# Optimization experiments

Hardware: AMD Instinct MI355X
Metric: run time of the kernel (lower is better)

## Reference

```python
import jax, jax.numpy as jnp
import numpy as np

B, S, D_IN, D_Q, D_K = 4, 4096, 1024, 128, 128


def setup_inputs() -> dict:
    key = jax.random.key(0)
    ks = jax.random.split(key, 9)
    inv = 1.0 / np.sqrt(D_IN)
    return {
        "query": jax.random.normal(ks[0], (B, S, D_IN), dtype=jnp.float32),
        "key": jax.random.normal(ks[1], (B, S, D_IN), dtype=jnp.float32),
        "value": jax.random.normal(ks[2], (B, S, D_IN), dtype=jnp.float32),
        "Wq": jax.random.uniform(ks[3], (D_IN, D_Q), jnp.float32, -inv, inv),
        "bq": jax.random.uniform(ks[4], (D_Q,), jnp.float32, -inv, inv),
        "Wk": jax.random.uniform(ks[5], (D_IN, D_K), jnp.float32, -inv, inv),
        "bk": jax.random.uniform(ks[6], (D_K,), jnp.float32, -inv, inv),
        "Wv": jax.random.uniform(ks[7], (D_IN, D_K), jnp.float32, -inv, inv),
        "bv": jax.random.uniform(ks[8], (D_K,), jnp.float32, -inv, inv),
    }


def reference(query, key, value, Wq, bq, Wk, bk, Wv, bv):
    q = query @ Wq + bq          # [B,S,Dq]
    k = key @ Wk + bk            # [B,S,Dk]
    v = value @ Wv + bv          # [B,S,Dk]
    scale = 1.0 / jnp.sqrt(jnp.asarray(q.shape[-1], q.dtype))
    logits = jnp.einsum('bqd,bkd->bqk', q, k) * scale  # [B,S,S]
    attn = jax.nn.softmax(logits, axis=-1)
    return jnp.einsum('bqk,bkd->bqd', attn, v)         # [B,S,Dk]
```

## Files before the change

kernel.cpp:

```cpp
#include <hip/hip_runtime.h>
#include <hip/hip_bf16.h>


typedef __attribute__((ext_vector_type(8))) short v8s;
typedef __attribute__((ext_vector_type(4))) float v4f;
typedef __attribute__((ext_vector_type(2))) unsigned int v2u;
typedef __attribute__((ext_vector_type(4))) int v4i;

#define SEQ   4096
#define DIN   1024
#define DH    128
#define NBAT  4

__device__ __forceinline__ unsigned short f2bf(float f) {
  unsigned u = __float_as_uint(f);
  u += 0x7fffu + ((u >> 16) & 1u);
  return (unsigned short)(u >> 16);
}

__global__ void prep_weights(const float* __restrict__ Wq, const float* __restrict__ Wk,
                             const float* __restrict__ Wv, short* __restrict__ Wt) {
  int idx = blockIdx.x * 256 + threadIdx.x;
  int z = idx >> 17;
  int e = idx & 131071;
  int k = e >> 7, c = e & 127;
  const float* W = (z == 0) ? Wq : (z == 1) ? Wk : Wv;
  Wt[z * 131072 + c * 1024 + k] = (short)f2bf(W[e]);
}

__global__ __launch_bounds__(256) void qkv_proj(
    const float* __restrict__ Xq, const float* __restrict__ Xk, const float* __restrict__ Xv,
    const float* __restrict__ bq, const float* __restrict__ bk, const float* __restrict__ bv,
    const short* __restrict__ Wt,
    short* __restrict__ Qb, short* __restrict__ Kb, short* __restrict__ Vtb) {
  const int z = blockIdx.y;
  const float* X    = (z == 0) ? Xq : (z == 1) ? Xk : Xv;
  const float* bias = (z == 0) ? bq : (z == 1) ? bk : bv;
  const short* W    = Wt + z * 131072;

  const int tid = threadIdx.x, wid = tid >> 6, lane = tid & 63;
  const int lg = lane >> 4, li = lane & 15;
  const int r0 = blockIdx.x * 128 + wid * 32;

  const float* xp0 = X + (size_t)(r0 + li) * DIN + lg * 8;
  const float* xp1 = xp0 + (size_t)16 * DIN;

  v4f acc[2][8];
#pragma unroll
  for (int mi = 0; mi < 2; ++mi)
#pragma unroll
    for (int ni = 0; ni < 8; ++ni) { acc[mi][ni][0]=0.f; acc[mi][ni][1]=0.f; acc[mi][ni][2]=0.f; acc[mi][ni][3]=0.f; }

#pragma unroll 2
  for (int ks = 0; ks < 32; ++ks) {
    v4f x0 = *(const v4f*)(xp0 + ks * 32);
    v4f x1 = *(const v4f*)(xp0 + ks * 32 + 4);
    v4f y0 = *(const v4f*)(xp1 + ks * 32);
    v4f y1 = *(const v4f*)(xp1 + ks * 32 + 4);
    v8s a0, a1;
    a0[0]=(short)f2bf(x0[0]); a0[1]=(short)f2bf(x0[1]); a0[2]=(short)f2bf(x0[2]); a0[3]=(short)f2bf(x0[3]);
    a0[4]=(short)f2bf(x1[0]); a0[5]=(short)f2bf(x1[1]); a0[6]=(short)f2bf(x1[2]); a0[7]=(short)f2bf(x1[3]);
    a1[0]=(short)f2bf(y0[0]); a1[1]=(short)f2bf(y0[1]); a1[2]=(short)f2bf(y0[2]); a1[3]=(short)f2bf(y0[3]);
    a1[4]=(short)f2bf(y1[0]); a1[5]=(short)f2bf(y1[1]); a1[6]=(short)f2bf(y1[2]); a1[7]=(short)f2bf(y1[3]);
#pragma unroll
    for (int ni = 0; ni < 8; ++ni) {
      v8s b = *(const v8s*)&W[(ni * 16 + li) * DIN + ks * 32 + lg * 8];
      acc[0][ni] = __builtin_amdgcn_mfma_f32_16x16x32_bf16(a0, b, acc[0][ni], 0, 0, 0);
      acc[1][ni] = __builtin_amdgcn_mfma_f32_16x16x32_bf16(a1, b, acc[1][ni], 0, 0, 0);
    }
  }

#pragma unroll
  for (int ni = 0; ni < 8; ++ni) {
    const int col = ni * 16 + li;
    const float bb = bias[col];
#pragma unroll
    for (int mi = 0; mi < 2; ++mi) {
      const int row0 = r0 + mi * 16 + lg * 4;
      v4f r = acc[mi][ni];
      if (z < 2) {
        short* Out = (z == 0) ? Qb : Kb;
#pragma unroll
        for (int rr = 0; rr < 4; ++rr)
          Out[(size_t)(row0 + rr) * DH + col] = (short)f2bf(r[rr] + bb);
      } else {
        const int bat = row0 >> 12;
        const int s0  = row0 & 4095;
        unsigned lo = (unsigned)f2bf(r[0] + bb) | ((unsigned)f2bf(r[1] + bb) << 16);
        unsigned hi = (unsigned)f2bf(r[2] + bb) | ((unsigned)f2bf(r[3] + bb) << 16);
        v2u pk; pk[0] = lo; pk[1] = hi;
        *(v2u*)&Vtb[(size_t)bat * (DH * SEQ) + (size_t)col * SEQ + s0] = pk;
      }
    }
  }
}

template <int NSPLIT>
__global__ __launch_bounds__(256) void attn_fwd(
    const short* __restrict__ Qb, const short* __restrict__ Kb, const short* __restrict__ Vtb,
    float* __restrict__ out, float* __restrict__ Opart,
    float* __restrict__ Mpart, float* __restrict__ Lpart) {
  constexpr int SLEN = SEQ / NSPLIT;
  constexpr int NT = SLEN / 64;
  __shared__ __align__(16) short Kl[2][64 * 128];
  __shared__ __align__(16) short Vl[2][128 * 64];
  __shared__ __align__(16) short Pl[4][32 * 64];

  const int tid = threadIdx.x, wid = tid >> 6, lane = tid & 63;
  const int lg = lane >> 4, li = lane & 15;
  const int b = blockIdx.y;
  const int sp = (NSPLIT > 1) ? blockIdx.z : 0;
  const int q0 = blockIdx.x * 128 + wid * 32;
  const float kSc = 0.08838834764831845f * 1.4426950408889634f;
  const int swz = (li & 7) << 4;

  const char* Kp = (const char*)(Kb + ((size_t)b * SEQ + (size_t)sp * SLEN) * DH);
  const char* Vp = (const char*)(Vtb + (size_t)b * (DH * SEQ) + (size_t)sp * SLEN);
  const short* Q = Qb + ((size_t)b * SEQ + q0) * DH;
  char* myP = (char*)&Pl[wid][0];

  v8s qf[4][2];
#pragma unroll
  for (int dc = 0; dc < 4; ++dc)
#pragma unroll
    for (int qh = 0; qh < 2; ++qh)
      qf[dc][qh] = *(const v8s*)&Q[(size_t)(qh * 16 + li) * DH + dc * 32 + lg * 8];

  v4f o[8][2];
#pragma unroll
  for (int dt = 0; dt < 8; ++dt)
#pragma unroll
    for (int qh = 0; qh < 2; ++qh) { o[dt][qh][0]=0.f; o[dt][qh][1]=0.f; o[dt][qh][2]=0.f; o[dt][qh][3]=0.f; }
  float m[2] = {-1e30f, -1e30f}, l[2] = {0.f, 0.f};

  v4i kreg[4], vreg[4];
  auto loadKV = [&](int st0) {
#pragma unroll
    for (int j = 0; j < 4; ++j) {
      int c = tid + j * 256;
      kreg[j] = *(const v4i*)(Kp + (size_t)st0 * 256 + c * 16);
    }
#pragma unroll
    for (int j = 0; j < 4; ++j) {
      int c = tid + j * 256;
      int d = c >> 3;
      vreg[j] = *(const v4i*)(Vp + (size_t)d * (SEQ * 2) + st0 * 2 + (c & 7) * 16);
    }
  };
  auto writeKV = [&](int buf) {
    char* kb = (char*)&Kl[buf][0];
    char* vb = (char*)&Vl[buf][0];
#pragma unroll
    for (int j = 0; j < 4; ++j) {
      int lin = (tid + j * 256) * 16;
      *(v4i*)(kb + (lin ^ (((lin >> 8) & 7) << 4))) = kreg[j];
    }
#pragma unroll
    for (int j = 0; j < 4; ++j) {
      int lin = (tid + j * 256) * 16;
      *(v4i*)(vb + (lin ^ (((lin >> 7) & 7) << 4))) = vreg[j];
    }
  };

  loadKV(0);
  writeKV(0);

#pragma unroll 1
  for (int t = 0; t < NT; ++t) {
    __syncthreads();
    const int buf = t & 1;
    if (t + 1 < NT) loadKV((t + 1) * 64);
    const char* kb = (const char*)&Kl[buf][0];
    const char* vb = (const char*)&Vl[buf][0];

    v4f stt[4][2];
#pragma unroll
    for (int tt = 0; tt < 4; ++tt)
#pragma unroll
      for (int qh = 0; qh < 2; ++qh) { stt[tt][qh][0]=0.f; stt[tt][qh][1]=0.f; stt[tt][qh][2]=0.f; stt[tt][qh][3]=0.f; }
#pragma unroll
    for (int tt = 0; tt < 4; ++tt)
#pragma unroll
      for (int dc = 0; dc < 4; ++dc) {
        v8s kf = *(const v8s*)(kb + ((((tt * 16 + li) * 256) + dc * 64 + lg * 16) ^ swz));
        stt[tt][0] = __builtin_amdgcn_mfma_f32_16x16x32_bf16(kf, qf[dc][0], stt[tt][0], 0, 0, 0);
        stt[tt][1] = __builtin_amdgcn_mfma_f32_16x16x32_bf16(kf, qf[dc][1], stt[tt][1], 0, 0, 0);
      }

    float fac[2];
#pragma unroll
    for (int qh = 0; qh < 2; ++qh) {
      float mx = m[qh];
#pragma unroll
      for (int tt = 0; tt < 4; ++tt)
        mx = fmaxf(mx, fmaxf(fmaxf(stt[tt][qh][0], stt[tt][qh][1]), fmaxf(stt[tt][qh][2], stt[tt][qh][3])));
      mx = fmaxf(mx, __shfl_xor(mx, 16));
      mx = fmaxf(mx, __shfl_xor(mx, 32));
      fac[qh] = exp2f((m[qh] - mx) * kSc);
      m[qh] = mx;
      float ps = 0.f;
#pragma unroll
      for (int tt = 0; tt < 4; ++tt) {
        float p0 = exp2f((stt[tt][qh][0] - mx) * kSc);
        float p1 = exp2f((stt[tt][qh][1] - mx) * kSc);
        float p2 = exp2f((stt[tt][qh][2] - mx) * kSc);
        float p3 = exp2f((stt[tt][qh][3] - mx) * kSc);
        ps += (p0 + p1) + (p2 + p3);
        v2u pk;
        pk[0] = (unsigned)f2bf(p0) | ((unsigned)f2bf(p1) << 16);
        pk[1] = (unsigned)f2bf(p2) | ((unsigned)f2bf(p3) << 16);
        *(v2u*)(myP + ((((qh * 16 + li) * 128) + tt * 32 + lg * 8) ^ swz)) = pk;
      }
      ps += __shfl_xor(ps, 16);
      ps += __shfl_xor(ps, 32);
      l[qh] = l[qh] * fac[qh] + ps;
    }

    float facr[2][4];
#pragma unroll
    for (int qh = 0; qh < 2; ++qh)
#pragma unroll
      for (int r = 0; r < 4; ++r) facr[qh][r] = __shfl(fac[qh], lg * 4 + r);
#pragma unroll
    for (int dt = 0; dt < 8; ++dt)
#pragma unroll
      for (int qh = 0; qh < 2; ++qh) {
        o[dt][qh][0] *= facr[qh][0]; o[dt][qh][1] *= facr[qh][1];
        o[dt][qh][2] *= facr[qh][2]; o[dt][qh][3] *= facr[qh][3];
      }

#pragma unroll
    for (int kk = 0; kk < 2; ++kk) {
      v8s pf0 = *(const v8s*)(myP + (((li * 128) + kk * 64 + lg * 16) ^ swz));
      v8s pf1 = *(const v8s*)(myP + ((((16 + li) * 128) + kk * 64 + lg * 16) ^ swz));
#pragma unroll
      for (int dt = 0; dt < 8; ++dt) {
        v8s vf = *(const v8s*)(vb + ((((dt * 16 + li) * 128) + kk * 64 + lg * 16) ^ swz));
        o[dt][0] = __builtin_amdgcn_mfma_f32_16x16x32_bf16(pf0, vf, o[dt][0], 0, 0, 0);
        o[dt][1] = __builtin_amdgcn_mfma_f32_16x16x32_bf16(pf1, vf, o[dt][1], 0, 0, 0);
      }
    }

    if (t + 1 < NT) writeKV(buf ^ 1);
  }

  float lr[2][4];
#pragma unroll
  for (int qh = 0; qh < 2; ++qh)
#pragma unroll
    for (int r = 0; r < 4; ++r) lr[qh][r] = __shfl(l[qh], lg * 4 + r);

  if (NSPLIT == 1) {
#pragma unroll
    for (int dt = 0; dt < 8; ++dt)
#pragma unroll
      for (int qh = 0; qh < 2; ++qh)
#pragma unroll
        for (int r = 0; r < 4; ++r)
          out[((size_t)b * SEQ + q0 + qh * 16 + lg * 4 + r) * DH + dt * 16 + li] =
              o[dt][qh][r] / lr[qh][r];
  } else {
    const size_t rb = ((size_t)sp * NBAT + b) * SEQ + q0;
#pragma unroll
    for (int dt = 0; dt < 8; ++dt)
#pragma unroll
      for (int qh = 0; qh < 2; ++qh)
#pragma unroll
        for (int r = 0; r < 4; ++r)
          Opart[(rb + qh * 16 + lg * 4 + r) * DH + dt * 16 + li] = o[dt][qh][r];
    if (lg == 0) {
#pragma unroll
      for (int qh = 0; qh < 2; ++qh) {
        Mpart[rb + qh * 16 + li] = m[qh];
        Lpart[rb + qh * 16 + li] = l[qh];
      }
    }
  }
}

template <int NSPLIT>
__global__ void merge_out(const float* __restrict__ Opart, const float* __restrict__ Mpart,
                          const float* __restrict__ Lpart, float* __restrict__ out) {
  const float kSc = 0.08838834764831845f * 1.4426950408889634f;
  int idx = blockIdx.x * 256 + threadIdx.x;
  int row = idx >> 7;
  float M = -1e30f;
#pragma unroll
  for (int zz = 0; zz < NSPLIT; ++zz) M = fmaxf(M, Mpart[zz * (NBAT * SEQ) + row]);
  float num = 0.f, den = 0.f;
#pragma unroll
  for (int zz = 0; zz < NSPLIT; ++zz) {
    float w = exp2f((Mpart[zz * (NBAT * SEQ) + row] - M) * kSc);
    num += w * Opart[(size_t)zz * ((size_t)NBAT * SEQ * DH) + idx];
    den += w * Lpart[zz * (NBAT * SEQ) + row];
  }
  out[idx] = num / den;
}

extern "C" void kernel_launch(void* const* d_in, const int* in_sizes, int n_in,
                              void* d_out, int out_size, void* d_ws, size_t ws_size,
                              hipStream_t stream) {
  const float* query = (const float*)d_in[0];
  const float* key   = (const float*)d_in[1];
  const float* value = (const float*)d_in[2];
  const float* Wq    = (const float*)d_in[3];
  const float* bqp   = (const float*)d_in[4];
  const float* Wk    = (const float*)d_in[5];
  const float* bkp   = (const float*)d_in[6];
  const float* Wv    = (const float*)d_in[7];
  const float* bvp   = (const float*)d_in[8];

  char* ws = (char*)d_ws;
  const size_t WT_SZ  = (size_t)3 * 128 * 1024 * 2;
  const size_t QKV_SZ = (size_t)NBAT * SEQ * DH * 2;
  short* Wt  = (short*)ws;
  short* Qb  = (short*)(ws + WT_SZ);
  short* Kb  = (short*)(ws + WT_SZ + QKV_SZ);
  short* Vtb = (short*)(ws + WT_SZ + 2 * QKV_SZ);
  char*  ext = ws + WT_SZ + 3 * QKV_SZ;
  const size_t OP4 = (size_t)4 * NBAT * SEQ * DH * 4;
  const size_t ST4 = (size_t)4 * NBAT * SEQ * 4;
  const size_t OP2 = OP4 / 2, ST2 = ST4 / 2;
  const size_t need4 = WT_SZ + 3 * QKV_SZ + OP4 + 2 * ST4;
  const size_t need2 = WT_SZ + 3 * QKV_SZ + OP2 + 2 * ST2;

  prep_weights<<<1536, 256, 0, stream>>>(Wq, Wk, Wv, Wt);
  qkv_proj<<<dim3(128, 3), 256, 0, stream>>>(query, key, value, bqp, bkp, bvp,
                                             Wt, Qb, Kb, Vtb);
  if (ws_size >= need4) {
    float* Opart = (float*)ext;
    float* Mpart = (float*)(ext + OP4);
    float* Lpart = (float*)(ext + OP4 + ST4);
    attn_fwd<4><<<dim3(32, NBAT, 4), 256, 0, stream>>>(Qb, Kb, Vtb, nullptr, Opart, Mpart, Lpart);
    merge_out<4><<<8192, 256, 0, stream>>>(Opart, Mpart, Lpart, (float*)d_out);
  } else if (ws_size >= need2) {
    float* Opart = (float*)ext;
    float* Mpart = (float*)(ext + OP2);
    float* Lpart = (float*)(ext + OP2 + ST2);
    attn_fwd<2><<<dim3(32, NBAT, 2), 256, 0, stream>>>(Qb, Kb, Vtb, nullptr, Opart, Mpart, Lpart);
    merge_out<2><<<8192, 256, 0, stream>>>(Opart, Mpart, Lpart, (float*)d_out);
  } else {
    attn_fwd<1><<<dim3(32, NBAT, 1), 256, 0, stream>>>(Qb, Kb, Vtb, (float*)d_out,
                                                       nullptr, nullptr, nullptr);
  }
}
```

Baseline: 393.1 us.

## Split keys across waves inside attention block and merge partials in LDS

```diff
diff --git a/kernel.cpp b/kernel.cpp
--- a/kernel.cpp
+++ b/kernel.cpp
@@ -40,33 +40,25 @@
 
   const int tid = threadIdx.x, wid = tid >> 6, lane = tid & 63;
   const int lg = lane >> 4, li = lane & 15;
-  const int r0 = blockIdx.x * 128 + wid * 32;
+  const int r0 = blockIdx.x * 64 + wid * 16;
 
   const float* xp0 = X + (size_t)(r0 + li) * DIN + lg * 8;
-  const float* xp1 = xp0 + (size_t)16 * DIN;
-
-  v4f acc[2][8];
-#pragma unroll
-  for (int mi = 0; mi < 2; ++mi)
-#pragma unroll
-    for (int ni = 0; ni < 8; ++ni) { acc[mi][ni][0]=0.f; acc[mi][ni][1]=0.f; acc[mi][ni][2]=0.f; acc[mi][ni][3]=0.f; }
+
+  v4f acc[8];
+#pragma unroll
+  for (int ni = 0; ni < 8; ++ni) { acc[ni][0]=0.f; acc[ni][1]=0.f; acc[ni][2]=0.f; acc[ni][3]=0.f; }
 
 #pragma unroll 2
   for (int ks = 0; ks < 32; ++ks) {
     v4f x0 = *(const v4f*)(xp0 + ks * 32);
     v4f x1 = *(const v4f*)(xp0 + ks * 32 + 4);
-    v4f y0 = *(const v4f*)(xp1 + ks * 32);
-    v4f y1 = *(const v4f*)(xp1 + ks * 32 + 4);
-    v8s a0, a1;
+    v8s a0;
     a0[0]=(short)f2bf(x0[0]); a0[1]=(short)f2bf(x0[1]); a0[2]=(short)f2bf(x0[2]); a0[3]=(short)f2bf(x0[3]);
     a0[4]=(short)f2bf(x1[0]); a0[5]=(short)f2bf(x1[1]); a0[6]=(short)f2bf(x1[2]); a0[7]=(short)f2bf(x1[3]);
-    a1[0]=(short)f2bf(y0[0]); a1[1]=(short)f2bf(y0[1]); a1[2]=(short)f2bf(y0[2]); a1[3]=(short)f2bf(y0[3]);
-    a1[4]=(short)f2bf(y1[0]); a1[5]=(short)f2bf(y1[1]); a1[6]=(short)f2bf(y1[2]); a1[7]=(short)f2bf(y1[3]);
 #pragma unroll
     for (int ni = 0; ni < 8; ++ni) {
       v8s b = *(const v8s*)&W[(ni * 16 + li) * DIN + ks * 32 + lg * 8];
-      acc[0][ni] = __builtin_amdgcn_mfma_f32_16x16x32_bf16(a0, b, acc[0][ni], 0, 0, 0);
-      acc[1][ni] = __builtin_amdgcn_mfma_f32_16x16x32_bf16(a1, b, acc[1][ni], 0, 0, 0);
+      acc[ni] = __builtin_amdgcn_mfma_f32_16x16x32_bf16(a0, b, acc[ni], 0, 0, 0);
     }
   }
 
@@ -74,50 +66,41 @@
   for (int ni = 0; ni < 8; ++ni) {
     const int col = ni * 16 + li;
     const float bb = bias[col];
-#pragma unroll
-    for (int mi = 0; mi < 2; ++mi) {
-      const int row0 = r0 + mi * 16 + lg * 4;
-      v4f r = acc[mi][ni];
-      if (z < 2) {
-        short* Out = (z == 0) ? Qb : Kb;
-#pragma unroll
-        for (int rr = 0; rr < 4; ++rr)
-          Out[(size_t)(row0 + rr) * DH + col] = (short)f2bf(r[rr] + bb);
-      } else {
-        const int bat = row0 >> 12;
-        const int s0  = row0 & 4095;
-        unsigned lo = (unsigned)f2bf(r[0] + bb) | ((unsigned)f2bf(r[1] + bb) << 16);
-        unsigned hi = (unsigned)f2bf(r[2] + bb) | ((unsigned)f2bf(r[3] + bb) << 16);
-        v2u pk; pk[0] = lo; pk[1] = hi;
-        *(v2u*)&Vtb[(size_t)bat * (DH * SEQ) + (size_t)col * SEQ + s0] = pk;
-      }
-    }
-  }
-}
-
-template <int NSPLIT>
-__global__ __launch_bounds__(256) void attn_fwd(
-    const short* __restrict__ Qb, const short* __restrict__ Kb, const short* __restrict__ Vtb,
-    float* __restrict__ out, float* __restrict__ Opart,
-    float* __restrict__ Mpart, float* __restrict__ Lpart) {
-  constexpr int SLEN = SEQ / NSPLIT;
-  constexpr int NT = SLEN / 64;
-  __shared__ __align__(16) short Kl[2][64 * 128];
-  __shared__ __align__(16) short Vl[2][128 * 64];
-  __shared__ __align__(16) short Pl[4][32 * 64];
-
-  const int tid = threadIdx.x, wid = tid >> 6, lane = tid & 63;
+    const int row0 = r0 + lg * 4;
+    v4f r = acc[ni];
+    if (z < 2) {
+      short* Out = (z == 0) ? Qb : Kb;
+#pragma unroll
+      for (int rr = 0; rr < 4; ++rr)
+        Out[(size_t)(row0 + rr) * DH + col] = (short)f2bf(r[rr] + bb);
+    } else {
+      const int bat = row0 >> 12;
+      const int s0  = row0 & 4095;
+      unsigned lo = (unsigned)f2bf(r[0] + bb) | ((unsigned)f2bf(r[1] + bb) << 16);
+      unsigned hi = (unsigned)f2bf(r[2] + bb) | ((unsigned)f2bf(r[3] + bb) << 16);
+      v2u pk; pk[0] = lo; pk[1] = hi;
+      *(v2u*)&Vtb[(size_t)bat * (DH * SEQ) + (size_t)col * SEQ + s0] = pk;
+    }
+  }
+}
+
+__global__ __launch_bounds__(512, 2) void attn_fwd(
+    const short* __restrict__ Qb, const short* __restrict__ Kb,
+    const short* __restrict__ Vtb, float* __restrict__ out) {
+  __shared__ __align__(16) char lds[133120];
+
+  const int tid = threadIdx.x, w = tid >> 6, lane = tid & 63;
   const int lg = lane >> 4, li = lane & 15;
   const int b = blockIdx.y;
-  const int sp = (NSPLIT > 1) ? blockIdx.z : 0;
-  const int q0 = blockIdx.x * 128 + wid * 32;
+  const int q0 = blockIdx.x * 32;
   const float kSc = 0.08838834764831845f * 1.4426950408889634f;
-  const int swz = (li & 7) << 4;
-
-  const char* Kp = (const char*)(Kb + ((size_t)b * SEQ + (size_t)sp * SLEN) * DH);
-  const char* Vp = (const char*)(Vtb + (size_t)b * (DH * SEQ) + (size_t)sp * SLEN);
-  const short* Q = Qb + ((size_t)b * SEQ + q0) * DH;
-  char* myP = (char*)&Pl[wid][0];
+
+  char* Klds = lds + w * 10240;
+  char* Plds = Klds + 8192;
+
+  const short* Q  = Qb + ((size_t)b * SEQ + q0) * DH;
+  const char* Kp  = (const char*)(Kb + ((size_t)b * SEQ + w * 512) * DH);
+  const char* Vpc = (const char*)Vtb + ((size_t)b * DH * SEQ + w * 512) * 2;
 
   v8s qf[4][2];
 #pragma unroll
@@ -133,66 +116,53 @@
     for (int qh = 0; qh < 2; ++qh) { o[dt][qh][0]=0.f; o[dt][qh][1]=0.f; o[dt][qh][2]=0.f; o[dt][qh][3]=0.f; }
   float m[2] = {-1e30f, -1e30f}, l[2] = {0.f, 0.f};
 
-  v4i kreg[4], vreg[4];
-  auto loadKV = [&](int st0) {
-#pragma unroll
-    for (int j = 0; j < 4; ++j) {
-      int c = tid + j * 256;
-      kreg[j] = *(const v4i*)(Kp + (size_t)st0 * 256 + c * 16);
-    }
-#pragma unroll
-    for (int j = 0; j < 4; ++j) {
-      int c = tid + j * 256;
-      int d = c >> 3;
-      vreg[j] = *(const v4i*)(Vp + (size_t)d * (SEQ * 2) + st0 * 2 + (c & 7) * 16);
-    }
+  const int krow = lane >> 1, khalf = lane & 1;
+  v4i kreg[8];
+  auto loadK = [&](int st) {
+    const char* p = Kp + (size_t)st * 8192 + krow * 256 + khalf * 128;
+#pragma unroll
+    for (int j = 0; j < 8; ++j) kreg[j] = *(const v4i*)(p + j * 16);
   };
-  auto writeKV = [&](int buf) {
-    char* kb = (char*)&Kl[buf][0];
-    char* vb = (char*)&Vl[buf][0];
-#pragma unroll
-    for (int j = 0; j < 4; ++j) {
-      int lin = (tid + j * 256) * 16;
-      *(v4i*)(kb + (lin ^ (((lin >> 8) & 7) << 4))) = kreg[j];
-    }
-#pragma unroll
-    for (int j = 0; j < 4; ++j) {
-      int lin = (tid + j * 256) * 16;
-      *(v4i*)(vb + (lin ^ (((lin >> 7) & 7) << 4))) = vreg[j];
+  auto writeK = [&]() {
+#pragma unroll
+    for (int j = 0; j < 8; ++j) {
+      int c = krow * 256 + khalf * 128 + j * 16;
+      *(v4i*)(Klds + (c ^ ((krow & 7) << 4))) = kreg[j];
     }
   };
 
-  loadKV(0);
-  writeKV(0);
+  loadK(0);
+  writeK();
 
 #pragma unroll 1
-  for (int t = 0; t < NT; ++t) {
-    __syncthreads();
-    const int buf = t & 1;
-    if (t + 1 < NT) loadKV((t + 1) * 64);
-    const char* kb = (const char*)&Kl[buf][0];
-    const char* vb = (const char*)&Vl[buf][0];
-
-    v4f stt[4][2];
-#pragma unroll
-    for (int tt = 0; tt < 4; ++tt)
+  for (int t = 0; t < 16; ++t) {
+    if (t < 15) loadK(t + 1);
+
+    v4f stt[2][2];
+#pragma unroll
+    for (int tt = 0; tt < 2; ++tt)
 #pragma unroll
       for (int qh = 0; qh < 2; ++qh) { stt[tt][qh][0]=0.f; stt[tt][qh][1]=0.f; stt[tt][qh][2]=0.f; stt[tt][qh][3]=0.f; }
 #pragma unroll
-    for (int tt = 0; tt < 4; ++tt)
+    for (int tt = 0; tt < 2; ++tt)
 #pragma unroll
       for (int dc = 0; dc < 4; ++dc) {
-        v8s kf = *(const v8s*)(kb + ((((tt * 16 + li) * 256) + dc * 64 + lg * 16) ^ swz));
+        v8s kf = *(const v8s*)(Klds + ((((tt * 16 + li) * 256) + dc * 64 + lg * 16) ^ ((li & 7) << 4)));
         stt[tt][0] = __builtin_amdgcn_mfma_f32_16x16x32_bf16(kf, qf[dc][0], stt[tt][0], 0, 0, 0);
         stt[tt][1] = __builtin_amdgcn_mfma_f32_16x16x32_bf16(kf, qf[dc][1], stt[tt][1], 0, 0, 0);
       }
 
+    v8s vf[8];
+#pragma unroll
+    for (int dt = 0; dt < 8; ++dt)
+      vf[dt] = *(const v8s*)(Vpc + (size_t)(dt * 16 + li) * 8192 + (size_t)t * 64 + lg * 16);
+
     float fac[2];
 #pragma unroll
     for (int qh = 0; qh < 2; ++qh) {
       float mx = m[qh];
 #pragma unroll
-      for (int tt = 0; tt < 4; ++tt)
+      for (int tt = 0; tt < 2; ++tt)
         mx = fmaxf(mx, fmaxf(fmaxf(stt[tt][qh][0], stt[tt][qh][1]), fmaxf(stt[tt][qh][2], stt[tt][qh][3])));
       mx = fmaxf(mx, __shfl_xor(mx, 16));
       mx = fmaxf(mx, __shfl_xor(mx, 32));
@@ -200,7 +170,7 @@
       m[qh] = mx;
       float ps = 0.f;
 #pragma unroll
-      for (int tt = 0; tt < 4; ++tt) {
+      for (int tt = 0; tt < 2; ++tt) {
         float p0 = exp2f((stt[tt][qh][0] - mx) * kSc);
         float p1 = exp2f((stt[tt][qh][1] - mx) * kSc);
         float p2 = exp2f((stt[tt][qh][2] - mx) * kSc);
@@ -209,13 +179,15 @@
         v2u pk;
         pk[0] = (unsigned)f2bf(p0) | ((unsigned)f2bf(p1) << 16);
         pk[1] = (unsigned)f2bf(p2) | ((unsigned)f2bf(p3) << 16);
-        *(v2u*)(myP + ((((qh * 16 + li) * 128) + tt * 32 + lg * 8) ^ swz)) = pk;
+        *(v2u*)(Plds + ((((qh * 16 + li) * 64) + tt * 32 + lg * 8) ^ ((li & 3) << 4))) = pk;
       }
       ps += __shfl_xor(ps, 16);
       ps += __shfl_xor(ps, 32);
       l[qh] = l[qh] * fac[qh] + ps;
     }
 
+    if (t < 15) writeK();
+
     float facr[2][4];
 #pragma unroll
     for (int qh = 0; qh < 2; ++qh)
@@ -229,72 +201,55 @@
         o[dt][qh][2] *= facr[qh][2]; o[dt][qh][3] *= facr[qh][3];
       }
 
-#pragma unroll
-    for (int kk = 0; kk < 2; ++kk) {
-      v8s pf0 = *(const v8s*)(myP + (((li * 128) + kk * 64 + lg * 16) ^ swz));
-      v8s pf1 = *(const v8s*)(myP + ((((16 + li) * 128) + kk * 64 + lg * 16) ^ swz));
-#pragma unroll
-      for (int dt = 0; dt < 8; ++dt) {
-        v8s vf = *(const v8s*)(vb + ((((dt * 16 + li) * 128) + kk * 64 + lg * 16) ^ swz));
-        o[dt][0] = __builtin_amdgcn_mfma_f32_16x16x32_bf16(pf0, vf, o[dt][0], 0, 0, 0);
-        o[dt][1] = __builtin_amdgcn_mfma_f32_16x16x32_bf16(pf1, vf, o[dt][1], 0, 0, 0);
-      }
-    }
-
-    if (t + 1 < NT) writeKV(buf ^ 1);
-  }
-
-  float lr[2][4];
-#pragma unroll
-  for (int qh = 0; qh < 2; ++qh)
-#pragma unroll
-    for (int r = 0; r < 4; ++r) lr[qh][r] = __shfl(l[qh], lg * 4 + r);
-
-  if (NSPLIT == 1) {
-#pragma unroll
-    for (int dt = 0; dt < 8; ++dt)
-#pragma unroll
-      for (int qh = 0; qh < 2; ++qh)
-#pragma unroll
-        for (int r = 0; r < 4; ++r)
-          out[((size_t)b * SEQ + q0 + qh * 16 + lg * 4 + r) * DH + dt * 16 + li] =
-              o[dt][qh][r] / lr[qh][r];
-  } else {
-    const size_t rb = ((size_t)sp * NBAT + b) * SEQ + q0;
-#pragma unroll
-    for (int dt = 0; dt < 8; ++dt)
-#pragma unroll
-      for (int qh = 0; qh < 2; ++qh)
-#pragma unroll
-        for (int r = 0; r < 4; ++r)
-          Opart[(rb + qh * 16 + lg * 4 + r) * DH + dt * 16 + li] = o[dt][qh][r];
-    if (lg == 0) {
-#pragma unroll
-      for (int qh = 0; qh < 2; ++qh) {
-        Mpart[rb + qh * 16 + li] = m[qh];
-        Lpart[rb + qh * 16 + li] = l[qh];
-      }
-    }
-  }
-}
-
-template <int NSPLIT>
-__global__ void merge_out(const float* __restrict__ Opart, const float* __restrict__ Mpart,
-                          const float* __restrict__ Lpart, float* __restrict__ out) {
-  const float kSc = 0.08838834764831845f * 1.4426950408889634f;
-  int idx = blockIdx.x * 256 + threadIdx.x;
-  int row = idx >> 7;
+    v8s pf[2];
+#pragma unroll
+    for (int qh = 0; qh < 2; ++qh)
+      pf[qh] = *(const v8s*)(Plds + ((((qh * 16 + li) * 64) + lg * 16) ^ ((li & 3) << 4)));
+#pragma unroll
+    for (int dt = 0; dt < 8; ++dt) {
+      o[dt][0] = __builtin_amdgcn_mfma_f32_16x16x32_bf16(pf[0], vf[dt], o[dt][0], 0, 0, 0);
+      o[dt][1] = __builtin_amdgcn_mfma_f32_16x16x32_bf16(pf[1], vf[dt], o[dt][1], 0, 0, 0);
+    }
+  }
+
+  float* olds = (float*)lds;
+  float* mlds = (float*)(lds + 131072);
+  float* llds = (float*)(lds + 132096);
+  __syncthreads();
+#pragma unroll
+  for (int dt = 0; dt < 8; ++dt)
+#pragma unroll
+    for (int qh = 0; qh < 2; ++qh)
+#pragma unroll
+      for (int r = 0; r < 4; ++r)
+        olds[w * 4096 + (qh * 16 + lg * 4 + r) * 128 + dt * 16 + li] = o[dt][qh][r];
+  if (lg == 0) {
+#pragma unroll
+    for (int qh = 0; qh < 2; ++qh) {
+      mlds[w * 32 + qh * 16 + li] = m[qh];
+      llds[w * 32 + qh * 16 + li] = l[qh];
+    }
+  }
+  __syncthreads();
+
+  const int q = tid >> 4, d0 = (tid & 15) * 8;
   float M = -1e30f;
 #pragma unroll
-  for (int zz = 0; zz < NSPLIT; ++zz) M = fmaxf(M, Mpart[zz * (NBAT * SEQ) + row]);
-  float num = 0.f, den = 0.f;
-#pragma unroll
-  for (int zz = 0; zz < NSPLIT; ++zz) {
-    float w = exp2f((Mpart[zz * (NBAT * SEQ) + row] - M) * kSc);
-    num += w * Opart[(size_t)zz * ((size_t)NBAT * SEQ * DH) + idx];
-    den += w * Lpart[zz * (NBAT * SEQ) + row];
-  }
-  out[idx] = num / den;
+  for (int ww = 0; ww < 8; ++ww) M = fmaxf(M, mlds[ww * 32 + q]);
+  float den = 0.f;
+  float av[8] = {0.f, 0.f, 0.f, 0.f, 0.f, 0.f, 0.f, 0.f};
+#pragma unroll
+  for (int ww = 0; ww < 8; ++ww) {
+    float wt = exp2f((mlds[ww * 32 + q] - M) * kSc);
+    den += wt * llds[ww * 32 + q];
+    const float* op = &olds[ww * 4096 + q * 128 + d0];
+#pragma unroll
+    for (int j = 0; j < 8; ++j) av[j] += wt * op[j];
+  }
+  const float inv = 1.f / den;
+  float* dst = out + ((size_t)b * SEQ + q0 + q) * DH + d0;
+#pragma unroll
+  for (int j = 0; j < 8; ++j) dst[j] = av[j] * inv;
 }
 
 extern "C" void kernel_launch(void* const* d_in, const int* in_sizes, int n_in,
@@ -317,30 +272,9 @@
   short* Qb  = (short*)(ws + WT_SZ);
   short* Kb  = (short*)(ws + WT_SZ + QKV_SZ);
   short* Vtb = (short*)(ws + WT_SZ + 2 * QKV_SZ);
-  char*  ext = ws + WT_SZ + 3 * QKV_SZ;
-  const size_t OP4 = (size_t)4 * NBAT * SEQ * DH * 4;
-  const size_t ST4 = (size_t)4 * NBAT * SEQ * 4;
-  const size_t OP2 = OP4 / 2, ST2 = ST4 / 2;
-  const size_t need4 = WT_SZ + 3 * QKV_SZ + OP4 + 2 * ST4;
-  const size_t need2 = WT_SZ + 3 * QKV_SZ + OP2 + 2 * ST2;
 
   prep_weights<<<1536, 256, 0, stream>>>(Wq, Wk, Wv, Wt);
-  qkv_proj<<<dim3(128, 3), 256, 0, stream>>>(query, key, value, bqp, bkp, bvp,
+  qkv_proj<<<dim3(256, 3), 256, 0, stream>>>(query, key, value, bqp, bkp, bvp,
                                              Wt, Qb, Kb, Vtb);
-  if (ws_size >= need4) {
-    float* Opart = (float*)ext;
-    float* Mpart = (float*)(ext + OP4);
-    float* Lpart = (float*)(ext + OP4 + ST4);
-    attn_fwd<4><<<dim3(32, NBAT, 4), 256, 0, stream>>>(Qb, Kb, Vtb, nullptr, Opart, Mpart, Lpart);
-    merge_out<4><<<8192, 256, 0, stream>>>(Opart, Mpart, Lpart, (float*)d_out);
-  } else if (ws_size >= need2) {
-    float* Opart = (float*)ext;
-    float* Mpart = (float*)(ext + OP2);
-    float* Lpart = (float*)(ext + OP2 + ST2);
-    attn_fwd<2><<<dim3(32, NBAT, 2), 256, 0, stream>>>(Qb, Kb, Vtb, nullptr, Opart, Mpart, Lpart);
-    merge_out<2><<<8192, 256, 0, stream>>>(Opart, Mpart, Lpart, (float*)d_out);
-  } else {
-    attn_fwd<1><<<dim3(32, NBAT, 1), 256, 0, stream>>>(Qb, Kb, Vtb, (float*)d_out,
-                                                       nullptr, nullptr, nullptr);
-  }
-}
+  attn_fwd<<<dim3(128, NBAT), 512, 0, stream>>>(Qb, Kb, Vtb, (float*)d_out);
+}
```

After: 414.2 us. 5.4% more time.
